# Kernel optimization log

Hardware: AMD Instinct MI355X
Metric: run time of the kernel (lower is better)

The kernel has to match this reference:

```python
import jax, jax.numpy as jnp
import numpy as np

EPS = 1e-5  # torch LayerNorm default

def ln(x, g, b):
    mu = jnp.mean(x, axis=-1, keepdims=True)
    var = jnp.mean((x - mu) ** 2, axis=-1, keepdims=True)
    return (x - mu) * jax.lax.rsqrt(var + EPS) * g + b

B, S, E, A = 131072, 199, 3, 32
D_IN = S + 1  # state_dim + 1 (time feature)

def setup_inputs() -> dict:
    key = jax.random.key(0)
    ks = iter(jax.random.split(key, 32))
    def w(shape, fan_in):
        lim = 1.0 / np.sqrt(fan_in)
        return jax.random.uniform(next(ks), shape, jnp.float32, -lim, lim)
    inp = {
        "state": jax.random.normal(next(ks), (B, S), jnp.float32),
        "time_delta": jax.random.uniform(next(ks), (B,), jnp.float32),
        # trunk: Linear(200,256)+LN, Linear(256,256)+LN, Linear(256,128)+LN
        "W1": w((D_IN, 256), D_IN), "b1": w((256,), D_IN),
        "g1": jnp.ones((256,), jnp.float32), "be1": jnp.zeros((256,), jnp.float32),
        "W2": w((256, 256), 256), "b2": w((256,), 256),
        "g2": jnp.ones((256,), jnp.float32), "be2": jnp.zeros((256,), jnp.float32),
        "W3": w((256, 128), 256), "b3": w((128,), 256),
        "g3": jnp.ones((128,), jnp.float32), "be3": jnp.zeros((128,), jnp.float32),
        # value stream
        "Wv1": w((128, 64), 128), "bv1": w((64,), 128),
        "gv": jnp.ones((64,), jnp.float32), "bev": jnp.zeros((64,), jnp.float32),
        "Wv2": w((64, 1), 64), "bv2": w((1,), 64),
        # E stacked advantage streams (all heads share action dim A)
        "Wa1": w((E, 128, 64), 128), "ba1": w((E, 64), 128),
        "ga": jnp.ones((E, 64), jnp.float32), "bea": jnp.zeros((E, 64), jnp.float32),
        "Wa2": w((E, 64, A), 64), "ba2": w((E, A), 64),
        "event_type": jax.random.randint(next(ks), (B,), 0, E),
    }
    return inp

def reference(state, time_delta,
              W1, b1, g1, be1, W2, b2, g2, be2, W3, b3, g3, be3,
              Wv1, bv1, gv, bev, Wv2, bv2,
              Wa1, ba1, ga, bea, Wa2, ba2, event_type):
    td = time_delta[:, None]                       # [B,1]
    x = jnp.concatenate([state, td], axis=1)       # [B,200]
    h = jax.nn.relu(ln(x @ W1 + b1, g1, be1))      # [B,256]
    h = jax.nn.relu(ln(h @ W2 + b2, g2, be2))      # [B,256]
    f = jax.nn.relu(ln(h @ W3 + b3, g3, be3))      # [B,128]
    v = jax.nn.relu(ln(f @ Wv1 + bv1, gv, bev)) @ Wv2 + bv2  # [B,1]
    # compute all E advantage heads, then per-sample select by event_type
    h1 = jnp.einsum('bd,edh->ebh', f, Wa1) + ba1[:, None, :]           # [E,B,64]
    h1 = jax.nn.relu(ln(h1, ga[:, None, :], bea[:, None, :]))
    adv_all = jnp.einsum('ebh,eha->eba', h1, Wa2) + ba2[:, None, :]    # [E,B,A]
    adv = jnp.take_along_axis(adv_all, event_type[None, :, None], axis=0)[0]  # [B,A]
    return v + (adv - adv.mean(axis=1, keepdims=True))
```

## Files before the change

### kernel.cpp

```cpp
#include <hip/hip_runtime.h>
#include <hip/hip_bf16.h>
#include <stdint.h>

#define DEV __device__ __forceinline__

typedef __attribute__((ext_vector_type(8))) short short8;
typedef __attribute__((ext_vector_type(4))) float floatx4;

constexpr int TM  = 64;
constexpr int NB  = 131072;
constexpr int AST = 264;

constexpr int OFF_W1 = 0;
constexpr int OFF_W2 = 57344;
constexpr int OFF_W3 = 122880;
constexpr int OFF_WH = 155648;
constexpr int OFF_WA2= 188416;
constexpr int NWQ    = 194560;

constexpr int C_B1=0, C_G1=256, C_BE1=512, C_B2=768, C_G2=1024, C_BE2=1280,
  C_B3=1536, C_G3=1664, C_BE3=1792, C_BV1=1920, C_GV=1984, C_BEV=2048,
  C_WV2=2112, C_BV2=2176, C_BA1=2180, C_GA=2372, C_BEA=2564, C_BA2=2756;
constexpr int NCONST=2852;

struct Ptrs {
  const float *state,*td,*W1,*b1,*g1,*be1,*W2,*b2,*g2,*be2,*W3,*b3,*g3,*be3,
    *Wv1,*bv1,*gv,*bev,*Wv2,*bv2,*Wa1,*ba1,*ga,*bea,*Wa2,*ba2;
  const int *et;
};

DEV unsigned short f2bf(float x){
  uint32_t u = __float_as_uint(x);
  u += 0x7fffu + ((u>>16)&1u);
  return (unsigned short)(u>>16);
}
DEV uint32_t f2bf_pk(float a, float b){
  float2 f2; f2.x=a; f2.y=b;
  __hip_bfloat162 h = __float22bfloat162_rn(f2);
  union { __hip_bfloat162 h; uint32_t u; } cv; cv.h = h;
  return cv.u;
}

DEV void keep8(const short8 &v){ asm volatile("" :: "v"(v)); }

__global__ void prep_kernel(Ptrs p, unsigned short* __restrict__ wq, float* __restrict__ cq){
  int idx = blockIdx.x*256 + threadIdx.x;
  if (idx < NWQ) {
    float v = 0.f;
    if (idx < OFF_W2) {
      int e = idx, w = e/14336, r = e%14336;
      int kc = r>>11, ct=(r>>9)&3, l=(r>>3)&63, j=r&7;
      int n = w*64 + ct*16 + (l&15);
      int k = kc*32 + (l>>4)*8 + j;
      if (k < 200) v = p.W1[k*256 + n];
      else if (k == 200) v = p.b1[n];
    } else if (idx < OFF_W3) {
      int e = idx-OFF_W2, w=e>>14, r=e&16383;
      int kc=r>>11, ct=(r>>9)&3, l=(r>>3)&63, j=r&7;
      int n = w*64 + ct*16 + (l&15);
      int k = kc*32 + (l>>4)*8 + j;
      v = p.W2[k*256 + n];
    } else if (idx < OFF_WH) {
      int e = idx-OFF_W3, w=e>>13, r=e&8191;
      int kc=r>>10, ct=(r>>9)&1, l=(r>>3)&63, j=r&7;
      int n = w*32 + ct*16 + (l&15);
      int k = kc*32 + (l>>4)*8 + j;
      v = p.W3[k*128 + n];
    } else if (idx < OFF_WA2) {
      int e = idx-OFF_WH, h=e>>13, r=e&8191;
      int kc=r>>11, ct=(r>>9)&3, l=(r>>3)&63, j=r&7;
      int n = ct*16 + (l&15);
      int k = kc*32 + (l>>4)*8 + j;
      v = (h<3) ? p.Wa1[h*8192 + k*64 + n] : p.Wv1[k*64 + n];
    } else {
      int e = idx-OFF_WA2, h=e>>11, r=e&2047;
      int kc=r>>10, ct=(r>>9)&1, l=(r>>3)&63, j=r&7;
      int n = ct*16 + (l&15);
      int k = kc*32 + (l>>4)*8 + j;
      v = p.Wa2[h*2048 + k*32 + n];
    }
    wq[idx] = f2bf(v);
  } else if (idx < NWQ + NCONST) {
    int ci = idx - NWQ;
    float v;
    if      (ci < 256)  v = p.b1[ci];
    else if (ci < 512)  v = p.g1[ci-256];
    else if (ci < 768)  v = p.be1[ci-512];
    else if (ci < 1024) v = p.b2[ci-768];
    else if (ci < 1280) v = p.g2[ci-1024];
    else if (ci < 1536) v = p.be2[ci-1280];
    else if (ci < 1664) v = p.b3[ci-1536];
    else if (ci < 1792) v = p.g3[ci-1664];
    else if (ci < 1920) v = p.be3[ci-1792];
    else if (ci < 1984) v = p.bv1[ci-1920];
    else if (ci < 2048) v = p.gv[ci-1984];
    else if (ci < 2112) v = p.bev[ci-2048];
    else if (ci < 2176) v = p.Wv2[ci-2112];
    else if (ci < 2180) v = (ci==2176) ? p.bv2[0] : 0.f;
    else if (ci < 2372) v = p.ba1[ci-2180];
    else if (ci < 2564) v = p.ga[ci-2372];
    else if (ci < 2756) v = p.bea[ci-2564];
    else                v = p.ba2[ci-2756];
    cq[ci] = v;
  }
}

template<int RT>
DEV void zeroAccT(floatx4 (&acc)[RT][4]){
  const floatx4 z = {0.f,0.f,0.f,0.f};
  #pragma unroll
  for (int rt=0;rt<RT;rt++)
    #pragma unroll
    for (int ct=0;ct<4;ct++) acc[rt][ct]=z;
}

template<int KC,int RT>
DEV void runGemmP(floatx4 (&acc)[RT][4], const unsigned short* __restrict__ wp,
                  const unsigned short* __restrict__ aB, int aOff, int lane,
                  const short8 (&pf)[4]){
  #pragma unroll
  for (int kc=0;kc<KC;kc++){
    short8 a[4];
    #pragma unroll
    for (int c=0;c<4;c++)
      a[c] = *(const short8*)(aB + c*16*AST + aOff + kc*32);
    #pragma unroll
    for (int rt=0;rt<RT;rt++){
      short8 bw;
      if constexpr (true){
        if (kc*RT+rt < 4) bw = pf[kc*RT+rt];
        else bw = *(const short8*)(wp + (kc*RT+rt)*512 + lane*8);
      }
      #pragma unroll
      for (int c=0;c<4;c++)
        acc[rt][c] = __builtin_amdgcn_mfma_f32_16x16x32_bf16(bw, a[c], acc[rt][c], 0,0,0);
    }
  }
}

template<int RT,bool BIAS>
DEV void statsS(floatx4 (&acc)[RT][4], const float* __restrict__ cq, int bo,
                float (&sst)[2][64][4], int w, int q, int ln){
  if constexpr (BIAS){
    #pragma unroll
    for (int rt=0;rt<RT;rt++){
      floatx4 b4 = *(const floatx4*)(cq + bo + rt*16 + q*4);
      #pragma unroll
      for (int ct=0;ct<4;ct++) acc[rt][ct] += b4;
    }
  }
  #pragma unroll
  for (int ct=0;ct<4;ct++){
    float s=0.f, ss=0.f;
    #pragma unroll
    for (int rt=0;rt<RT;rt++)
      #pragma unroll
      for (int r=0;r<4;r++){ float v=acc[rt][ct][r]; s+=v; ss+=v*v; }
    s += __shfl_xor(s,16); ss += __shfl_xor(ss,16);
    s += __shfl_xor(s,32); ss += __shfl_xor(ss,32);
    if (q==0){
      sst[0][ct*16+ln][w] = s;
      sst[1][ct*16+ln][w] = ss;
    }
  }
}

template<int RT>
DEV void lnWriteS(const floatx4 (&acc)[RT][4], const float* __restrict__ cq, int go, int beo,
                  const float (&sst)[2][64][4], float invN,
                  unsigned short* act_, int colBase, int q, int ln){
  float mu[4], rs[4];
  #pragma unroll
  for (int ct=0;ct<4;ct++){
    int row = ct*16+ln;
    floatx4 s4 = *(const floatx4*)&sst[0][row][0];
    floatx4 q4 = *(const floatx4*)&sst[1][row][0];
    float sv = (s4[0]+s4[1])+(s4[2]+s4[3]);
    float qv = (q4[0]+q4[1])+(q4[2]+q4[3]);
    mu[ct] = sv*invN;
    rs[ct] = rsqrtf(qv*invN - mu[ct]*mu[ct] + 1e-5f);
  }
  #pragma unroll
  for (int rt=0;rt<RT;rt++){
    floatx4 g4  = *(const floatx4*)(cq + go  + rt*16 + q*4);
    floatx4 be4 = *(const floatx4*)(cq + beo + rt*16 + q*4);
    #pragma unroll
    for (int ct=0;ct<4;ct++){
      float y[4];
      #pragma unroll
      for (int r=0;r<4;r++)
        y[r] = fmaxf((acc[rt][ct][r]-mu[ct])*rs[ct]*g4[r]+be4[r], 0.f);
      uint2 pk; pk.x = f2bf_pk(y[0],y[1]); pk.y = f2bf_pk(y[2],y[3]);
      *(uint2*)(act_ + (ct*16+ln)*AST + colBase + rt*16 + q*4) = pk;
    }
  }
}

__global__ __launch_bounds__(256,4) void dqn_main(
    const float* __restrict__ state, const float* __restrict__ td,
    const int* __restrict__ et, const unsigned short* __restrict__ wq,
    const float* __restrict__ cq, float* __restrict__ out)
{
  __shared__ __align__(16) unsigned short act[TM*AST];
  __shared__ __align__(16) float sstat[2][64][4];
  __shared__ float vbuf[64];
  __shared__ int   etl[64];

  const int tid=threadIdx.x, w=tid>>6, lane=tid&63, q=lane>>4, ln=lane&15;
  const int rowBlk = blockIdx.x*TM;

  const unsigned short* wl1 = wq + OFF_W1 + w*14336;
  const unsigned short* wl2 = wq + OFF_W2 + w*16384;
  const unsigned short* wl3 = wq + OFF_W3 + w*8192;
  const unsigned short* wlh = wq + OFF_WH + w*8192;
  const unsigned short* aBase = act + ln*AST + q*8;

  short8 pf[4];

  #pragma unroll
  for (int i=0;i<4;i++) pf[i] = *(const short8*)(wl1 + i*512 + lane*8);

  {
    const float* sbase = state + (size_t)rowBlk*199;
    #pragma unroll
    for (int it=0; it<7; ++it){
      int t = tid + it*256;
      int r = t/28, c = t - r*28;
      unsigned short* dst = act + r*AST + c*8;
      if (c < 25){
        const float* src = sbase + r*199 + c*8;
        float v0=src[0], v1=src[1], v2=src[2], v3=src[3];
        float v4=src[4], v5=src[5], v6=src[6];
        int o7 = (c==24)? 198 : c*8+7;
        float s7 = sbase[r*199 + o7];
        float v7 = (c==24)? td[rowBlk+r] : s7;
        uint4 pk;
        pk.x=f2bf_pk(v0,v1); pk.y=f2bf_pk(v2,v3);
        pk.z=f2bf_pk(v4,v5); pk.w=f2bf_pk(v6,v7);
        *(uint4*)dst = pk;
      } else {
        uint4 pk{0u,0u,0u,0u};
        if (c==25) pk.x = 0x3F80u;
        *(uint4*)dst = pk;
      }
    }
    if (tid < 64) etl[tid] = et[rowBlk+tid];
  }
  #pragma unroll
  for (int i=0;i<4;i++) keep8(pf[i]);
  __syncthreads();

  floatx4 acc[4][4];

  zeroAccT<4>(acc);
  runGemmP<7,4>(acc, wl1, aBase, 0, lane, pf);
  statsS<4,false>(acc, cq, 0, sstat, w, q, ln);
  __syncthreads();

  #pragma unroll
  for (int i=0;i<4;i++) pf[i] = *(const short8*)(wl2 + i*512 + lane*8);
  lnWriteS<4>(acc, cq, C_G1+w*64, C_BE1+w*64, sstat, 1.f/256.f, act, w*64, q, ln);
  #pragma unroll
  for (int i=0;i<4;i++) keep8(pf[i]);
  __syncthreads();

  zeroAccT<4>(acc);
  runGemmP<8,4>(acc, wl2, aBase, 0, lane, pf);
  statsS<4,true>(acc, cq, C_B2+w*64, sstat, w, q, ln);
  __syncthreads();

  #pragma unroll
  for (int i=0;i<4;i++) pf[i] = *(const short8*)(wl3 + i*512 + lane*8);
  lnWriteS<4>(acc, cq, C_G2+w*64, C_BE2+w*64, sstat, 1.f/256.f, act, w*64, q, ln);
  #pragma unroll
  for (int i=0;i<4;i++) keep8(pf[i]);
  __syncthreads();

  floatx4 acc3[2][4];
  zeroAccT<2>(acc3);
  runGemmP<8,2>(acc3, wl3, aBase, 0, lane, pf);
  statsS<2,true>(acc3, cq, C_B3+w*32, sstat, w, q, ln);
  __syncthreads();

  #pragma unroll
  for (int i=0;i<4;i++) pf[i] = *(const short8*)(wlh + i*512 + lane*8);
  lnWriteS<2>(acc3, cq, C_G3+w*32, C_BE3+w*32, sstat, 1.f/128.f, act, w*32, q, ln);
  #pragma unroll
  for (int i=0;i<4;i++) keep8(pf[i]);
  __syncthreads();

  short8 pfa[4];
  if (w<3){
    #pragma unroll
    for (int i=0;i<4;i++)
      pfa[i] = *(const short8*)(wq + OFF_WA2 + w*2048 + i*512 + lane*8);
  }
  zeroAccT<4>(acc);
  runGemmP<4,4>(acc, wlh, aBase, 0, lane, pf);
  {
    const int bo = (w<3)? C_BA1+w*64 : C_BV1;
    const int go = (w<3)? C_GA +w*64 : C_GV;
    const int beo= (w<3)? C_BEA+w*64 : C_BEV;
    #pragma unroll
    for (int rt=0;rt<4;rt++){
      floatx4 b4 = *(const floatx4*)(cq + bo + rt*16 + q*4);
      #pragma unroll
      for (int ct=0;ct<4;ct++) acc[rt][ct] += b4;
    }
    float mu[4], rs[4];
    #pragma unroll
    for (int ct=0;ct<4;ct++){
      float s=0.f, ss=0.f;
      #pragma unroll
      for (int rt=0;rt<4;rt++)
        #pragma unroll
        for (int r=0;r<4;r++){ float v=acc[rt][ct][r]; s+=v; ss+=v*v; }
      s += __shfl_xor(s,16); ss += __shfl_xor(ss,16);
      s += __shfl_xor(s,32); ss += __shfl_xor(ss,32);
      mu[ct]=s*(1.f/64.f);
      rs[ct]=rsqrtf(ss*(1.f/64.f)-mu[ct]*mu[ct]+1e-5f);
    }
    #pragma unroll
    for (int rt=0;rt<4;rt++){
      floatx4 g4  = *(const floatx4*)(cq + go  + rt*16 + q*4);
      floatx4 be4 = *(const floatx4*)(cq + beo + rt*16 + q*4);
      #pragma unroll
      for (int ct=0;ct<4;ct++)
        #pragma unroll
        for (int r=0;r<4;r++)
          acc[rt][ct][r] = fmaxf((acc[rt][ct][r]-mu[ct])*rs[ct]*g4[r]+be4[r], 0.f);
    }
    if (w==3){
      float bv2v = cq[C_BV2];
      floatx4 wv4[4];
      #pragma unroll
      for (int rt=0;rt<4;rt++) wv4[rt] = *(const floatx4*)(cq + C_WV2 + rt*16 + q*4);
      #pragma unroll
      for (int ct=0;ct<4;ct++){
        float dot=0.f;
        #pragma unroll
        for (int rt=0;rt<4;rt++)
          #pragma unroll
          for (int r=0;r<4;r++) dot += acc[rt][ct][r]*wv4[rt][r];
        dot += __shfl_xor(dot,16);
        dot += __shfl_xor(dot,32);
        if (q==0) vbuf[ct*16+ln] = dot + bv2v;
      }
    }
  }
  if (w<3){
    #pragma unroll
    for (int i=0;i<4;i++) keep8(pfa[i]);
  }
  __syncthreads();

  if (w<3){
    #pragma unroll
    for (int rt=0;rt<4;rt++)
      #pragma unroll
      for (int ct=0;ct<4;ct++){
        uint2 pk;
        pk.x = f2bf_pk(acc[rt][ct][0], acc[rt][ct][1]);
        pk.y = f2bf_pk(acc[rt][ct][2], acc[rt][ct][3]);
        *(uint2*)(act + (ct*16+ln)*AST + 64*w + rt*16 + q*4) = pk;
      }
    floatx4 acc2[2][4];
    zeroAccT<2>(acc2);
    #pragma unroll
    for (int kc=0;kc<2;kc++){
      short8 a[4];
      #pragma unroll
      for (int c=0;c<4;c++)
        a[c] = *(const short8*)(aBase + c*16*AST + 64*w + kc*32);
      #pragma unroll
      for (int rt=0;rt<2;rt++)
        #pragma unroll
        for (int c=0;c<4;c++)
          acc2[rt][c] = __builtin_amdgcn_mfma_f32_16x16x32_bf16(pfa[kc*2+rt], a[c], acc2[rt][c], 0,0,0);
    }
    #pragma unroll
    for (int rt=0;rt<2;rt++){
      floatx4 b4 = *(const floatx4*)(cq + C_BA2 + w*32 + rt*16 + q*4);
      #pragma unroll
      for (int ct=0;ct<4;ct++) acc2[rt][ct] += b4;
    }
    #pragma unroll
    for (int ct=0;ct<4;ct++){
      float sm=0.f;
      #pragma unroll
      for (int rt=0;rt<2;rt++)
        #pragma unroll
        for (int r=0;r<4;r++) sm += acc2[rt][ct][r];
      sm += __shfl_xor(sm,16);
      sm += __shfl_xor(sm,32);
      int b = ct*16+ln;
      if (etl[b]==w){
        float vm = vbuf[b] - sm*(1.f/32.f);
        #pragma unroll
        for (int rt=0;rt<2;rt++){
          floatx4 o = acc2[rt][ct];
          o[0]+=vm; o[1]+=vm; o[2]+=vm; o[3]+=vm;
          *(floatx4*)(out + (size_t)(rowBlk+b)*32 + rt*16 + q*4) = o;
        }
      }
    }
  }
}

extern "C" void kernel_launch(void* const* d_in, const int* in_sizes, int n_in,
                              void* d_out, int out_size, void* d_ws, size_t ws_size,
                              hipStream_t stream)
{
  Ptrs p;
  p.state=(const float*)d_in[0];  p.td =(const float*)d_in[1];
  p.W1 =(const float*)d_in[2];  p.b1 =(const float*)d_in[3];  p.g1 =(const float*)d_in[4];  p.be1=(const float*)d_in[5];
  p.W2 =(const float*)d_in[6];  p.b2 =(const float*)d_in[7];  p.g2 =(const float*)d_in[8];  p.be2=(const float*)d_in[9];
  p.W3 =(const float*)d_in[10]; p.b3 =(const float*)d_in[11]; p.g3 =(const float*)d_in[12]; p.be3=(const float*)d_in[13];
  p.Wv1=(const float*)d_in[14]; p.bv1=(const float*)d_in[15]; p.gv =(const float*)d_in[16]; p.bev=(const float*)d_in[17];
  p.Wv2=(const float*)d_in[18]; p.bv2=(const float*)d_in[19];
  p.Wa1=(const float*)d_in[20]; p.ba1=(const float*)d_in[21]; p.ga =(const float*)d_in[22]; p.bea=(const float*)d_in[23];
  p.Wa2=(const float*)d_in[24]; p.ba2=(const float*)d_in[25];
  p.et =(const int*)d_in[26];

  unsigned short* wq = (unsigned short*)d_ws;
  float* cq = (float*)((char*)d_ws + (size_t)NWQ*2);

  const int prepN = NWQ + NCONST;
  hipLaunchKernelGGL(prep_kernel, dim3((prepN+255)/256), dim3(256), 0, stream, p, wq, cq);
  hipLaunchKernelGGL(dqn_main, dim3(NB/TM), dim3(256), 0, stream,
                     p.state, p.td, p.et, (const unsigned short*)wq, (const float*)cq, (float*)d_out);
}
```

Baseline: 289.3 us.

## Drop weight prefetch registers, seed accumulators with bias, raise MFMA priority

Removes the cross-phase weight prefetch into registers (the pf/pfa arrays pinned with asm keep), so each GEMM now loads its B fragments directly from global memory inside the loop. Accumulators are initialised with the bias vector instead of zeroed and later bias-added. The GEMM loop is wrapped in s_setprio(1)/s_setprio(0) to favour the MFMA-issuing waves. This lowers register pressure and removes redundant adds, but gives up the latency hiding the prefetch offered across __syncthreads boundaries.

```diff
diff --git a/kernel.cpp b/kernel.cpp
--- a/kernel.cpp
+++ b/kernel.cpp
@@ -40,8 +40,6 @@
   union { __hip_bfloat162 h; uint32_t u; } cv; cv.h = h;
   return cv.u;
 }
-
-DEV void keep8(const short8 &v){ asm volatile("" :: "v"(v)); }
 
 __global__ void prep_kernel(Ptrs p, unsigned short* __restrict__ wq, float* __restrict__ cq){
   int idx = blockIdx.x*256 + threadIdx.x;
@@ -114,10 +112,20 @@
     for (int ct=0;ct<4;ct++) acc[rt][ct]=z;
 }
 
+template<int RT>
+DEV void biasAccT(floatx4 (&acc)[RT][4], const float* __restrict__ cqb, int q){
+  #pragma unroll
+  for (int rt=0;rt<RT;rt++){
+    floatx4 b4 = *(const floatx4*)(cqb + rt*16 + q*4);
+    #pragma unroll
+    for (int ct=0;ct<4;ct++) acc[rt][ct]=b4;
+  }
+}
+
 template<int KC,int RT>
-DEV void runGemmP(floatx4 (&acc)[RT][4], const unsigned short* __restrict__ wp,
-                  const unsigned short* __restrict__ aB, int aOff, int lane,
-                  const short8 (&pf)[4]){
+DEV void runGemmW(floatx4 (&acc)[RT][4], const unsigned short* __restrict__ wp,
+                  const unsigned short* __restrict__ aB, int aOff, int lane){
+  __builtin_amdgcn_s_setprio(1);
   #pragma unroll
   for (int kc=0;kc<KC;kc++){
     short8 a[4];
@@ -126,29 +134,18 @@
       a[c] = *(const short8*)(aB + c*16*AST + aOff + kc*32);
     #pragma unroll
     for (int rt=0;rt<RT;rt++){
-      short8 bw;
-      if constexpr (true){
-        if (kc*RT+rt < 4) bw = pf[kc*RT+rt];
-        else bw = *(const short8*)(wp + (kc*RT+rt)*512 + lane*8);
-      }
+      short8 bw = *(const short8*)(wp + (kc*RT+rt)*512 + lane*8);
       #pragma unroll
       for (int c=0;c<4;c++)
         acc[rt][c] = __builtin_amdgcn_mfma_f32_16x16x32_bf16(bw, a[c], acc[rt][c], 0,0,0);
     }
   }
-}
-
-template<int RT,bool BIAS>
-DEV void statsS(floatx4 (&acc)[RT][4], const float* __restrict__ cq, int bo,
+  __builtin_amdgcn_s_setprio(0);
+}
+
+template<int RT>
+DEV void statsS(const floatx4 (&acc)[RT][4],
                 float (&sst)[2][64][4], int w, int q, int ln){
-  if constexpr (BIAS){
-    #pragma unroll
-    for (int rt=0;rt<RT;rt++){
-      floatx4 b4 = *(const floatx4*)(cq + bo + rt*16 + q*4);
-      #pragma unroll
-      for (int ct=0;ct<4;ct++) acc[rt][ct] += b4;
-    }
-  }
   #pragma unroll
   for (int ct=0;ct<4;ct++){
     float s=0.f, ss=0.f;
@@ -214,11 +211,6 @@
   const unsigned short* wl3 = wq + OFF_W3 + w*8192;
   const unsigned short* wlh = wq + OFF_WH + w*8192;
   const unsigned short* aBase = act + ln*AST + q*8;
-
-  short8 pf[4];
-
-  #pragma unroll
-  for (int i=0;i<4;i++) pf[i] = *(const short8*)(wl1 + i*512 + lane*8);
 
   {
     const float* sbase = state + (size_t)rowBlk*199;
@@ -246,67 +238,38 @@
     }
     if (tid < 64) etl[tid] = et[rowBlk+tid];
   }
-  #pragma unroll
-  for (int i=0;i<4;i++) keep8(pf[i]);
   __syncthreads();
 
   floatx4 acc[4][4];
 
   zeroAccT<4>(acc);
-  runGemmP<7,4>(acc, wl1, aBase, 0, lane, pf);
-  statsS<4,false>(acc, cq, 0, sstat, w, q, ln);
-  __syncthreads();
-
-  #pragma unroll
-  for (int i=0;i<4;i++) pf[i] = *(const short8*)(wl2 + i*512 + lane*8);
+  runGemmW<7,4>(acc, wl1, aBase, 0, lane);
+  statsS<4>(acc, sstat, w, q, ln);
+  __syncthreads();
   lnWriteS<4>(acc, cq, C_G1+w*64, C_BE1+w*64, sstat, 1.f/256.f, act, w*64, q, ln);
-  #pragma unroll
-  for (int i=0;i<4;i++) keep8(pf[i]);
-  __syncthreads();
-
-  zeroAccT<4>(acc);
-  runGemmP<8,4>(acc, wl2, aBase, 0, lane, pf);
-  statsS<4,true>(acc, cq, C_B2+w*64, sstat, w, q, ln);
-  __syncthreads();
-
-  #pragma unroll
-  for (int i=0;i<4;i++) pf[i] = *(const short8*)(wl3 + i*512 + lane*8);
+  __syncthreads();
+
+  biasAccT<4>(acc, cq + C_B2 + w*64, q);
+  runGemmW<8,4>(acc, wl2, aBase, 0, lane);
+  statsS<4>(acc, sstat, w, q, ln);
+  __syncthreads();
   lnWriteS<4>(acc, cq, C_G2+w*64, C_BE2+w*64, sstat, 1.f/256.f, act, w*64, q, ln);
-  #pragma unroll
-  for (int i=0;i<4;i++) keep8(pf[i]);
   __syncthreads();
 
   floatx4 acc3[2][4];
-  zeroAccT<2>(acc3);
-  runGemmP<8,2>(acc3, wl3, aBase, 0, lane, pf);
-  statsS<2,true>(acc3, cq, C_B3+w*32, sstat, w, q, ln);
-  __syncthreads();
-
-  #pragma unroll
-  for (int i=0;i<4;i++) pf[i] = *(const short8*)(wlh + i*512 + lane*8);
+  biasAccT<2>(acc3, cq + C_B3 + w*32, q);
+  runGemmW<8,2>(acc3, wl3, aBase, 0, lane);
+  statsS<2>(acc3, sstat, w, q, ln);
+  __syncthreads();
   lnWriteS<2>(acc3, cq, C_G3+w*32, C_BE3+w*32, sstat, 1.f/128.f, act, w*32, q, ln);
-  #pragma unroll
-  for (int i=0;i<4;i++) keep8(pf[i]);
-  __syncthreads();
-
-  short8 pfa[4];
-  if (w<3){
-    #pragma unroll
-    for (int i=0;i<4;i++)
-      pfa[i] = *(const short8*)(wq + OFF_WA2 + w*2048 + i*512 + lane*8);
-  }
-  zeroAccT<4>(acc);
-  runGemmP<4,4>(acc, wlh, aBase, 0, lane, pf);
+  __syncthreads();
+
+  const int bo = (w<3)? C_BA1+w*64 : C_BV1;
+  const int go = (w<3)? C_GA +w*64 : C_GV;
+  const int beo= (w<3)? C_BEA+w*64 : C_BEV;
+  biasAccT<4>(acc, cq + bo, q);
+  runGemmW<4,4>(acc, wlh, aBase, 0, lane);
   {
-    const int bo = (w<3)? C_BA1+w*64 : C_BV1;
-    const int go = (w<3)? C_GA +w*64 : C_GV;
-    const int beo= (w<3)? C_BEA+w*64 : C_BEV;
-    #pragma unroll
-    for (int rt=0;rt<4;rt++){
-      floatx4 b4 = *(const floatx4*)(cq + bo + rt*16 + q*4);
-      #pragma unroll
-      for (int ct=0;ct<4;ct++) acc[rt][ct] += b4;
-    }
     float mu[4], rs[4];
     #pragma unroll
     for (int ct=0;ct<4;ct++){
@@ -348,10 +311,6 @@
       }
     }
   }
-  if (w<3){
-    #pragma unroll
-    for (int i=0;i<4;i++) keep8(pfa[i]);
-  }
   __syncthreads();
 
   if (w<3){
@@ -365,25 +324,8 @@
         *(uint2*)(act + (ct*16+ln)*AST + 64*w + rt*16 + q*4) = pk;
       }
     floatx4 acc2[2][4];
-    zeroAccT<2>(acc2);
-    #pragma unroll
-    for (int kc=0;kc<2;kc++){
-      short8 a[4];
-      #pragma unroll
-      for (int c=0;c<4;c++)
-        a[c] = *(const short8*)(aBase + c*16*AST + 64*w + kc*32);
-      #pragma unroll
-      for (int rt=0;rt<2;rt++)
-        #pragma unroll
-        for (int c=0;c<4;c++)
-          acc2[rt][c] = __builtin_amdgcn_mfma_f32_16x16x32_bf16(pfa[kc*2+rt], a[c], acc2[rt][c], 0,0,0);
-    }
-    #pragma unroll
-    for (int rt=0;rt<2;rt++){
-      floatx4 b4 = *(const floatx4*)(cq + C_BA2 + w*32 + rt*16 + q*4);
-      #pragma unroll
-      for (int ct=0;ct<4;ct++) acc2[rt][ct] += b4;
-    }
+    biasAccT<2>(acc2, cq + C_BA2 + w*32, q);
+    runGemmW<2,2>(acc2, wq + OFF_WA2 + w*2048, aBase, 64*w, lane);
     #pragma unroll
     for (int ct=0;ct<4;ct++){
       float sm=0.f;
```

Result: faster. 274.2 us (-5.2%).
